# Performance work log

Measured on AMD Instinct MI355X. Metric: run time of the kernel, lower is better.

The kernel has to match this reference:

```python
import jax, jax.numpy as jnp
import numpy as np

N, M, D = 16384, 16384, 64
BANDWIDTH = 10.0


def setup_inputs() -> dict:
    key = jax.random.key(0)
    k1, k2 = jax.random.split(key)
    points = jax.random.normal(k1, (M, D), dtype=jnp.float32)
    spatial_data = jax.random.normal(k2, (N, D), dtype=jnp.float32)
    weights = jnp.ones((N,), dtype=jnp.float32) / N
    bandwidth = jnp.float32(BANDWIDTH)
    return {"points": points, "spatial_data": spatial_data,
            "weights": weights, "bandwidth": bandwidth}


def reference(points, spatial_data, weights, bandwidth):
    # Squared Euclidean distances [M, N] via the GEMM expansion
    # ||p - s||^2 = ||p||^2 + ||s||^2 - 2 p.s  (clamped at 0 for fp safety)
    p_sq = jnp.sum(points * points, axis=-1, keepdims=True)        # [M, 1]
    s_sq = jnp.sum(spatial_data * spatial_data, axis=-1)           # [N]
    cross = jnp.einsum('md,nd->mn', points, spatial_data)          # [M, N]
    sq_dists = jnp.maximum(p_sq + s_sq[None, :] - 2.0 * cross, 0.0)
    # Gaussian RBF kernel: exp(-d^2 / (2 b^2)); cdist's sqrt then ** 2 cancel.
    kernels = jnp.exp(-sq_dists / (2.0 * bandwidth * bandwidth))   # [M, N]
    return jnp.sum(weights * kernels, axis=-1)                     # [M]
```

## Files before the change

kernel.cpp:

```cpp
#include <hip/hip_runtime.h>
#include <hip/hip_bf16.h>

#define M_PTS 16384
#define N_SPT 16384
#define DIM   64
#define NSL   16
#define SLN   (N_SPT / NSL)
#define BUFROWS 128
#define BUFBYTES (BUFROWS * DIM * 2)
#define ROUNDS (SLN / BUFROWS)
#define STEPS  (BUFROWS / 16)

typedef __attribute__((ext_vector_type(8))) short bf16x8;
typedef __attribute__((ext_vector_type(4))) float f32x4;

#define LOG2E 1.4426950408889634f

__device__ __forceinline__ unsigned short f32_bf16_rne(float f) {
  unsigned int x = __float_as_uint(f);
  x = x + 0x7fffu + ((x >> 16) & 1u);
  return (unsigned short)(x >> 16);
}
__device__ __forceinline__ float bf16_f32(unsigned short u) {
  return __uint_as_float(((unsigned int)u) << 16);
}

__global__ __launch_bounds__(256) void kde_prep(
    const float* __restrict__ pts, const float* __restrict__ spt,
    const float* __restrict__ w, const float* __restrict__ bw,
    unsigned short* __restrict__ ptsb, unsigned short* __restrict__ spb,
    float* __restrict__ Em, float* __restrict__ En) {
  const float b = bw[0];
  const float scale = LOG2E / (b * b);
  const float c1 = 0.5f * scale;
  const float invc = (b * b) / (2.0f * LOG2E);
  const int tid = threadIdx.x;
  const bool isP = blockIdx.x < (M_PTS / 16);
  const int r0 = isP ? (blockIdx.x * 16) : ((blockIdx.x - M_PTS / 16) * 16);
  const float* __restrict__ src = isP ? pts : spt;
  unsigned short* __restrict__ dst = isP ? ptsb : spb;

  size_t off = (size_t)r0 * DIM + (size_t)tid * 4;
  float4 v = *reinterpret_cast<const float4*>(src + off);
  if (isP) { v.x *= scale; v.y *= scale; v.z *= scale; v.w *= scale; }
  ushort4 u;
  u.x = f32_bf16_rne(v.x); u.y = f32_bf16_rne(v.y);
  u.z = f32_bf16_rne(v.z); u.w = f32_bf16_rne(v.w);
  float ax = bf16_f32(u.x), ay = bf16_f32(u.y);
  float az = bf16_f32(u.z), aw = bf16_f32(u.w);
  float sq = ax * ax + ay * ay + az * az + aw * aw;
  *reinterpret_cast<ushort4*>(dst + off) = u;

  sq += __shfl_xor(sq, 1);
  sq += __shfl_xor(sq, 2);
  sq += __shfl_xor(sq, 4);
  sq += __shfl_xor(sq, 8);
  if ((tid & 15) == 0) {
    int row = r0 + (tid >> 4);
    if (isP) Em[row] = exp2f(-sq * invc);
    else     En[row] = w[row] * exp2f(-sq * c1);
  }
}

__global__ __launch_bounds__(256) void kde_main(
    const unsigned short* __restrict__ ptsb,
    const unsigned short* __restrict__ spb,
    const float* __restrict__ En,
    float* __restrict__ partials) {
  __shared__ __align__(16) char ldsb[2 * BUFBYTES];
  __shared__ float lden[SLN];

  const int tid = threadIdx.x;
  const int lane = tid & 63;
  const int wave = tid >> 6;
  const int lr = lane & 15;
  const int lg = lane >> 4;
  const int mbase = blockIdx.x * 256 + wave * 64;
  const int s = blockIdx.y;

#pragma unroll
  for (int k = 0; k < SLN / 256; ++k)
    lden[tid + k * 256] = En[s * SLN + tid + k * 256];

  bf16x8 a[4][2];
#pragma unroll
  for (int t = 0; t < 4; ++t)
#pragma unroll
    for (int h = 0; h < 2; ++h)
      a[t][h] = *reinterpret_cast<const bf16x8*>(
          ptsb + (size_t)(mbase + t * 16 + lr) * DIM + h * 32 + lg * 8);

  const char* gbase = (const char*)spb + (size_t)s * SLN * DIM * 2;
  const int srcswz = ((lane >> 3) & 7) << 4;

#define STAGE(r, c)                                                          \
  {                                                                          \
    const char* g = gbase + (size_t)(r) * BUFBYTES;                          \
    _Pragma("unroll") for (int k = 0; k < 4; ++k) {                          \
      int P = wave * 4096 + k * 1024 + lane * 16;                            \
      char* ldst = ldsb + (c) * BUFBYTES + wave * 4096 + k * 1024;           \
      __builtin_amdgcn_global_load_lds(                                      \
          (const __attribute__((address_space(1))) void*)(g + (P ^ srcswz)), \
          (__attribute__((address_space(3))) void*)ldst, 16, 0, 0);          \
    }                                                                        \
  }

#define MFMA_STEP(C, q0, q1, st)                                             \
  {                                                                          \
    bf16x8 b0 = *reinterpret_cast<const bf16x8*>((q0) + (st) * 2048);        \
    bf16x8 b1 = *reinterpret_cast<const bf16x8*>((q1) + (st) * 2048);        \
    _Pragma("unroll") for (int t = 0; t < 4; ++t) {                          \
      C[t] = f32x4{0.0f, 0.0f, 0.0f, 0.0f};                                  \
      C[t] = __builtin_amdgcn_mfma_f32_16x16x32_bf16(a[t][0], b0, C[t],      \
                                                     0, 0, 0);               \
      C[t] = __builtin_amdgcn_mfma_f32_16x16x32_bf16(a[t][1], b1, C[t],      \
                                                     0, 0, 0);               \
    }                                                                        \
  }

#define FINISH(C, enr, st)                                                   \
  {                                                                          \
    float en = (enr)[(st) * 16];                                             \
    _Pragma("unroll") for (int t = 0; t < 4; ++t) {                          \
      _Pragma("unroll") for (int rr = 0; rr < 4; ++rr) {                     \
        float e;                                                             \
        asm("v_exp_f32 %0, %1" : "=v"(e) : "v"(C[t][rr]));                   \
        sum[t][rr] = fmaf(en, e, sum[t][rr]);                                \
      }                                                                      \
    }                                                                        \
  }

  float sum[4][4] = {{0.0f, 0.0f, 0.0f, 0.0f}, {0.0f, 0.0f, 0.0f, 0.0f},
                     {0.0f, 0.0f, 0.0f, 0.0f}, {0.0f, 0.0f, 0.0f, 0.0f}};

  const int swz = (lr & 7) << 4;
  const char* pb0 = ldsb + ((lr * 128 + lg * 16) ^ swz);
  const char* pb1 = ldsb + ((lr * 128 + 64 + lg * 16) ^ swz);

  STAGE(0, 0)
  asm volatile("s_waitcnt vmcnt(0)" ::: "memory");
  __syncthreads();

  for (int r = 0; r < ROUNDS; ++r) {
    if (r + 1 < ROUNDS) {
      STAGE(r + 1, (r + 1) & 1)
    }
    const char* q0 = pb0 + (r & 1) * BUFBYTES;
    const char* q1 = pb1 + (r & 1) * BUFBYTES;
    const float* enr = lden + r * BUFROWS + lr;

    f32x4 cA[4], cB[4];
    MFMA_STEP(cA, q0, q1, 0)
    MFMA_STEP(cB, q0, q1, 1) FINISH(cA, enr, 0)
    MFMA_STEP(cA, q0, q1, 2) FINISH(cB, enr, 1)
    MFMA_STEP(cB, q0, q1, 3) FINISH(cA, enr, 2)
    MFMA_STEP(cA, q0, q1, 4) FINISH(cB, enr, 3)
    MFMA_STEP(cB, q0, q1, 5) FINISH(cA, enr, 4)
    MFMA_STEP(cA, q0, q1, 6) FINISH(cB, enr, 5)
    MFMA_STEP(cB, q0, q1, 7) FINISH(cA, enr, 6)
    FINISH(cB, enr, 7)

    asm volatile("s_waitcnt vmcnt(0)" ::: "memory");
    __syncthreads();
  }
#undef STAGE
#undef MFMA_STEP
#undef FINISH

#pragma unroll
  for (int t = 0; t < 4; ++t)
#pragma unroll
    for (int r = 0; r < 4; ++r) {
      float v = sum[t][r];
      v += __shfl_xor(v, 1);
      v += __shfl_xor(v, 2);
      v += __shfl_xor(v, 4);
      v += __shfl_xor(v, 8);
      sum[t][r] = v;
    }
  if (lr == 0) {
#pragma unroll
    for (int t = 0; t < 4; ++t)
#pragma unroll
      for (int r = 0; r < 4; ++r) {
        int row = mbase + t * 16 + lg * 4 + r;
        partials[(size_t)s * M_PTS + row] = sum[t][r];
      }
  }
}

__global__ __launch_bounds__(256) void kde_reduce(
    const float* __restrict__ partials, const float* __restrict__ Em,
    float* __restrict__ out) {
  int m = blockIdx.x * 256 + threadIdx.x;
  float t = 0.0f;
#pragma unroll
  for (int s2 = 0; s2 < NSL; ++s2)
    t += partials[(size_t)s2 * M_PTS + m];
  out[m] = Em[m] * t;
}

extern "C" void kernel_launch(void* const* d_in, const int* in_sizes, int n_in,
                              void* d_out, int out_size, void* d_ws, size_t ws_size,
                              hipStream_t stream) {
  const float* pts = (const float*)d_in[0];
  const float* spt = (const float*)d_in[1];
  const float* w   = (const float*)d_in[2];
  const float* bw  = (const float*)d_in[3];
  float* out = (float*)d_out;

  char* ws = (char*)d_ws;
  unsigned short* ptsb = (unsigned short*)ws;
  unsigned short* spb  = (unsigned short*)(ws + (size_t)M_PTS * DIM * 2);
  float* Em = (float*)(ws + (size_t)(M_PTS + N_SPT) * DIM * 2);
  float* En = Em + M_PTS;
  float* partials = En + N_SPT;

  kde_prep<<<dim3((M_PTS + N_SPT) / 16), 256, 0, stream>>>(
      pts, spt, w, bw, ptsb, spb, Em, En);
  kde_main<<<dim3(M_PTS / 256, NSL), 256, 0, stream>>>(
      ptsb, spb, En, partials);
  kde_reduce<<<dim3(M_PTS / 256), 256, 0, stream>>>(partials, Em, out);
}
```

Measured before the change: 60.53 us.

## Load spatial tiles directly from global into registers and remap blocks across XCDs

Drops the LDS double buffer, the global_load_lds staging and the per-round barriers. Each lane now loads its B fragments straight from global memory into registers, software-pipelined one step ahead, and relies on L1/L2 to serve the four waves that read the same rows. The grid is flattened and block ids are remapped so that consecutive ids cycle through slices, giving each XCD a fixed pair of slices for better L2 locality. The risks are longer global-load latency exposed in the MFMA/exp loop and redundant per-wave fetches of identical data. The final prefetch also reads past the slice, which is harmless here because that data is never used.

```diff
diff --git a/kernel.cpp b/kernel.cpp
--- a/kernel.cpp
+++ b/kernel.cpp
@@ -6,10 +6,7 @@
 #define DIM   64
 #define NSL   16
 #define SLN   (N_SPT / NSL)
-#define BUFROWS 128
-#define BUFBYTES (BUFROWS * DIM * 2)
-#define ROUNDS (SLN / BUFROWS)
-#define STEPS  (BUFROWS / 16)
+#define TSTEPS (SLN / 16)
 
 typedef __attribute__((ext_vector_type(8))) short bf16x8;
 typedef __attribute__((ext_vector_type(4))) float f32x4;
@@ -67,7 +64,6 @@
     const unsigned short* __restrict__ spb,
     const float* __restrict__ En,
     float* __restrict__ partials) {
-  __shared__ __align__(16) char ldsb[2 * BUFBYTES];
   __shared__ float lden[SLN];
 
   const int tid = threadIdx.x;
@@ -75,8 +71,12 @@
   const int wave = tid >> 6;
   const int lr = lane & 15;
   const int lg = lane >> 4;
-  const int mbase = blockIdx.x * 256 + wave * 64;
-  const int s = blockIdx.y;
+
+  const int lid = blockIdx.x;
+  const int q = lid >> 3;
+  const int s = (lid & 7) * 2 + (q >> 6);
+  const int mb = q & 63;
+  const int mbase = mb * 256 + wave * 64;
 
 #pragma unroll
   for (int k = 0; k < SLN / 256; ++k)
@@ -90,37 +90,30 @@
       a[t][h] = *reinterpret_cast<const bf16x8*>(
           ptsb + (size_t)(mbase + t * 16 + lr) * DIM + h * 32 + lg * 8);
 
-  const char* gbase = (const char*)spb + (size_t)s * SLN * DIM * 2;
-  const int srcswz = ((lane >> 3) & 7) << 4;
-
-#define STAGE(r, c)                                                          \
+  __syncthreads();
+
+  const char* bptr =
+      (const char*)(spb + (size_t)s * SLN * DIM) + lr * 128 + lg * 16;
+  const float* enr = lden + lr;
+
+  const f32x4 kz = {0.0f, 0.0f, 0.0f, 0.0f};
+  float sum[4][4] = {{0.0f, 0.0f, 0.0f, 0.0f}, {0.0f, 0.0f, 0.0f, 0.0f},
+                     {0.0f, 0.0f, 0.0f, 0.0f}, {0.0f, 0.0f, 0.0f, 0.0f}};
+  f32x4 cA[4], cB[4];
+
+#define MS(C, B0, B1)                                                        \
   {                                                                          \
-    const char* g = gbase + (size_t)(r) * BUFBYTES;                          \
-    _Pragma("unroll") for (int k = 0; k < 4; ++k) {                          \
-      int P = wave * 4096 + k * 1024 + lane * 16;                            \
-      char* ldst = ldsb + (c) * BUFBYTES + wave * 4096 + k * 1024;           \
-      __builtin_amdgcn_global_load_lds(                                      \
-          (const __attribute__((address_space(1))) void*)(g + (P ^ srcswz)), \
-          (__attribute__((address_space(3))) void*)ldst, 16, 0, 0);          \
-    }                                                                        \
-  }
-
-#define MFMA_STEP(C, q0, q1, st)                                             \
-  {                                                                          \
-    bf16x8 b0 = *reinterpret_cast<const bf16x8*>((q0) + (st) * 2048);        \
-    bf16x8 b1 = *reinterpret_cast<const bf16x8*>((q1) + (st) * 2048);        \
     _Pragma("unroll") for (int t = 0; t < 4; ++t) {                          \
-      C[t] = f32x4{0.0f, 0.0f, 0.0f, 0.0f};                                  \
-      C[t] = __builtin_amdgcn_mfma_f32_16x16x32_bf16(a[t][0], b0, C[t],      \
+      C[t] = __builtin_amdgcn_mfma_f32_16x16x32_bf16(a[t][0], B0, kz,        \
                                                      0, 0, 0);               \
-      C[t] = __builtin_amdgcn_mfma_f32_16x16x32_bf16(a[t][1], b1, C[t],      \
+      C[t] = __builtin_amdgcn_mfma_f32_16x16x32_bf16(a[t][1], B1, C[t],      \
                                                      0, 0, 0);               \
     }                                                                        \
   }
 
-#define FINISH(C, enr, st)                                                   \
+#define FIN(C, EN)                                                           \
   {                                                                          \
-    float en = (enr)[(st) * 16];                                             \
+    float en = (EN);                                                         \
     _Pragma("unroll") for (int t = 0; t < 4; ++t) {                          \
       _Pragma("unroll") for (int rr = 0; rr < 4; ++rr) {                     \
         float e;                                                             \
@@ -130,42 +123,34 @@
     }                                                                        \
   }
 
-  float sum[4][4] = {{0.0f, 0.0f, 0.0f, 0.0f}, {0.0f, 0.0f, 0.0f, 0.0f},
-                     {0.0f, 0.0f, 0.0f, 0.0f}, {0.0f, 0.0f, 0.0f, 0.0f}};
-
-  const int swz = (lr & 7) << 4;
-  const char* pb0 = ldsb + ((lr * 128 + lg * 16) ^ swz);
-  const char* pb1 = ldsb + ((lr * 128 + 64 + lg * 16) ^ swz);
-
-  STAGE(0, 0)
-  asm volatile("s_waitcnt vmcnt(0)" ::: "memory");
-  __syncthreads();
-
-  for (int r = 0; r < ROUNDS; ++r) {
-    if (r + 1 < ROUNDS) {
-      STAGE(r + 1, (r + 1) & 1)
-    }
-    const char* q0 = pb0 + (r & 1) * BUFBYTES;
-    const char* q1 = pb1 + (r & 1) * BUFBYTES;
-    const float* enr = lden + r * BUFROWS + lr;
-
-    f32x4 cA[4], cB[4];
-    MFMA_STEP(cA, q0, q1, 0)
-    MFMA_STEP(cB, q0, q1, 1) FINISH(cA, enr, 0)
-    MFMA_STEP(cA, q0, q1, 2) FINISH(cB, enr, 1)
-    MFMA_STEP(cB, q0, q1, 3) FINISH(cA, enr, 2)
-    MFMA_STEP(cA, q0, q1, 4) FINISH(cB, enr, 3)
-    MFMA_STEP(cB, q0, q1, 5) FINISH(cA, enr, 4)
-    MFMA_STEP(cA, q0, q1, 6) FINISH(cB, enr, 5)
-    MFMA_STEP(cB, q0, q1, 7) FINISH(cA, enr, 6)
-    FINISH(cB, enr, 7)
-
-    asm volatile("s_waitcnt vmcnt(0)" ::: "memory");
-    __syncthreads();
-  }
-#undef STAGE
-#undef MFMA_STEP
-#undef FINISH
+  bf16x8 e0, e1, o0, o1;
+  e0 = *reinterpret_cast<const bf16x8*>(bptr);
+  e1 = *reinterpret_cast<const bf16x8*>(bptr + 64);
+  o0 = *reinterpret_cast<const bf16x8*>(bptr + 2048);
+  o1 = *reinterpret_cast<const bf16x8*>(bptr + 2048 + 64);
+
+  MS(cA, e0, e1)
+  e0 = *reinterpret_cast<const bf16x8*>(bptr + 2 * 2048);
+  e1 = *reinterpret_cast<const bf16x8*>(bptr + 2 * 2048 + 64);
+  MS(cB, o0, o1)
+  FIN(cA, enr[0])
+  o0 = *reinterpret_cast<const bf16x8*>(bptr + 3 * 2048);
+  o1 = *reinterpret_cast<const bf16x8*>(bptr + 3 * 2048 + 64);
+
+  const char* bp = bptr + 4 * 2048;
+  for (int u = 1; u < 32; ++u, bp += 2 * 2048) {
+    MS(cA, e0, e1)
+    FIN(cB, enr[(2 * u - 1) * 16])
+    e0 = *reinterpret_cast<const bf16x8*>(bp);
+    e1 = *reinterpret_cast<const bf16x8*>(bp + 64);
+    MS(cB, o0, o1)
+    FIN(cA, enr[(2 * u) * 16])
+    o0 = *reinterpret_cast<const bf16x8*>(bp + 2048);
+    o1 = *reinterpret_cast<const bf16x8*>(bp + 2048 + 64);
+  }
+  FIN(cB, enr[63 * 16])
+#undef MS
+#undef FIN
 
 #pragma unroll
   for (int t = 0; t < 4; ++t)
@@ -218,7 +203,7 @@
 
   kde_prep<<<dim3((M_PTS + N_SPT) / 16), 256, 0, stream>>>(
       pts, spt, w, bw, ptsb, spb, Em, En);
-  kde_main<<<dim3(M_PTS / 256, NSL), 256, 0, stream>>>(
+  kde_main<<<dim3(M_PTS / 256 * NSL), 256, 0, stream>>>(
       ptsb, spb, En, partials);
   kde_reduce<<<dim3(M_PTS / 256), 256, 0, stream>>>(partials, Em, out);
 }
```

Measured after the change: 89.06 us. 1.47x slower.

## Software-pipeline LDS B-fragment loads and defer staging past last reads

Applied to the files above, without the earlier changes.

Restructures the main loop so the LDS B-operand loads for the next MFMA step are issued one step ahead, using alternating register pairs. The next round's global-to-LDS staging moves to after the last LDS reads of the current buffer, and the first loads of the next buffer are issued right after the barrier, so the final exp/accumulate overlaps the barrier wait. It also feeds a constant zero accumulator to the first MFMA and fully unrolls the round loop. These changes aim to hide LDS and barrier latency behind MFMA and exp work, at the cost of more registers and larger code.

```diff
diff --git a/kernel.cpp b/kernel.cpp
--- a/kernel.cpp
+++ b/kernel.cpp
@@ -105,22 +105,27 @@
     }                                                                        \
   }
 
-#define MFMA_STEP(C, q0, q1, st)                                             \
+#define LDE(q0, q1, st)                                                      \
+  e0 = *reinterpret_cast<const bf16x8*>((q0) + (st) * 2048);                 \
+  e1 = *reinterpret_cast<const bf16x8*>((q1) + (st) * 2048);
+
+#define LDO(q0, q1, st)                                                      \
+  o0 = *reinterpret_cast<const bf16x8*>((q0) + (st) * 2048);                 \
+  o1 = *reinterpret_cast<const bf16x8*>((q1) + (st) * 2048);
+
+#define MS(C, B0, B1)                                                        \
   {                                                                          \
-    bf16x8 b0 = *reinterpret_cast<const bf16x8*>((q0) + (st) * 2048);        \
-    bf16x8 b1 = *reinterpret_cast<const bf16x8*>((q1) + (st) * 2048);        \
     _Pragma("unroll") for (int t = 0; t < 4; ++t) {                          \
-      C[t] = f32x4{0.0f, 0.0f, 0.0f, 0.0f};                                  \
-      C[t] = __builtin_amdgcn_mfma_f32_16x16x32_bf16(a[t][0], b0, C[t],      \
+      C[t] = __builtin_amdgcn_mfma_f32_16x16x32_bf16(a[t][0], B0, kz,        \
                                                      0, 0, 0);               \
-      C[t] = __builtin_amdgcn_mfma_f32_16x16x32_bf16(a[t][1], b1, C[t],      \
+      C[t] = __builtin_amdgcn_mfma_f32_16x16x32_bf16(a[t][1], B1, C[t],      \
                                                      0, 0, 0);               \
     }                                                                        \
   }
 
-#define FINISH(C, enr, st)                                                   \
+#define FINV(C, EN)                                                          \
   {                                                                          \
-    float en = (enr)[(st) * 16];                                             \
+    float en = (EN);                                                         \
     _Pragma("unroll") for (int t = 0; t < 4; ++t) {                          \
       _Pragma("unroll") for (int rr = 0; rr < 4; ++rr) {                     \
         float e;                                                             \
@@ -130,42 +135,70 @@
     }                                                                        \
   }
 
+#define FING(C, G) FINV(C, enp[(G) * 16])
+
+  const f32x4 kz = {0.0f, 0.0f, 0.0f, 0.0f};
   float sum[4][4] = {{0.0f, 0.0f, 0.0f, 0.0f}, {0.0f, 0.0f, 0.0f, 0.0f},
                      {0.0f, 0.0f, 0.0f, 0.0f}, {0.0f, 0.0f, 0.0f, 0.0f}};
+  f32x4 cA[4], cB[4];
+  bf16x8 e0, e1, o0, o1;
 
   const int swz = (lr & 7) << 4;
   const char* pb0 = ldsb + ((lr * 128 + lg * 16) ^ swz);
   const char* pb1 = ldsb + ((lr * 128 + 64 + lg * 16) ^ swz);
+  const float* enp = lden + lr;
 
   STAGE(0, 0)
   asm volatile("s_waitcnt vmcnt(0)" ::: "memory");
   __syncthreads();
 
+  LDE(pb0, pb1, 0)
+
+#pragma unroll
   for (int r = 0; r < ROUNDS; ++r) {
+    const char* q0 = pb0 + (r & 1) * BUFBYTES;
+    const char* q1 = pb1 + (r & 1) * BUFBYTES;
+
+    LDO(q0, q1, 1)
+    MS(cA, e0, e1)
+    LDE(q0, q1, 2)
+    MS(cB, o0, o1) FING(cA, r * 8 + 0)
+    LDO(q0, q1, 3)
+    MS(cA, e0, e1) FING(cB, r * 8 + 1)
+    LDE(q0, q1, 4)
+    MS(cB, o0, o1) FING(cA, r * 8 + 2)
+    LDO(q0, q1, 5)
+    MS(cA, e0, e1) FING(cB, r * 8 + 3)
+    LDE(q0, q1, 6)
+    MS(cB, o0, o1) FING(cA, r * 8 + 4)
+
+    float en5 = enp[(r * 8 + 5) * 16];
+    float en6 = enp[(r * 8 + 6) * 16];
+    float en7 = enp[(r * 8 + 7) * 16];
+    LDO(q0, q1, 7)
+
     if (r + 1 < ROUNDS) {
       STAGE(r + 1, (r + 1) & 1)
     }
-    const char* q0 = pb0 + (r & 1) * BUFBYTES;
-    const char* q1 = pb1 + (r & 1) * BUFBYTES;
-    const float* enr = lden + r * BUFROWS + lr;
-
-    f32x4 cA[4], cB[4];
-    MFMA_STEP(cA, q0, q1, 0)
-    MFMA_STEP(cB, q0, q1, 1) FINISH(cA, enr, 0)
-    MFMA_STEP(cA, q0, q1, 2) FINISH(cB, enr, 1)
-    MFMA_STEP(cB, q0, q1, 3) FINISH(cA, enr, 2)
-    MFMA_STEP(cA, q0, q1, 4) FINISH(cB, enr, 3)
-    MFMA_STEP(cB, q0, q1, 5) FINISH(cA, enr, 4)
-    MFMA_STEP(cA, q0, q1, 6) FINISH(cB, enr, 5)
-    MFMA_STEP(cB, q0, q1, 7) FINISH(cA, enr, 6)
-    FINISH(cB, enr, 7)
-
-    asm volatile("s_waitcnt vmcnt(0)" ::: "memory");
-    __syncthreads();
+
+    MS(cA, e0, e1) FINV(cB, en5)
+    MS(cB, o0, o1) FINV(cA, en6)
+
+    if (r + 1 < ROUNDS) {
+      asm volatile("s_waitcnt vmcnt(0)" ::: "memory");
+      __syncthreads();
+      const char* n0 = pb0 + ((r + 1) & 1) * BUFBYTES;
+      const char* n1 = pb1 + ((r + 1) & 1) * BUFBYTES;
+      LDE(n0, n1, 0)
+    }
+    FINV(cB, en7)
   }
 #undef STAGE
-#undef MFMA_STEP
-#undef FINISH
+#undef LDE
+#undef LDO
+#undef MS
+#undef FINV
+#undef FING
 
 #pragma unroll
   for (int t = 0; t < 4; ++t)
```

New measurement: 71.29 us. 1.18x slower.
